# Performance work log

Measured on AMD Instinct MI355X. Metric: run time of the kernel, lower is better.

## Reference

```python
import jax, jax.numpy as jnp
import numpy as np

B, T, C = 4, 2048, 1024
H, HD = 16, 64          # n_heads, head_dim (C = H*HD)
R = 8                   # LoRA rank
SCALING = 16.0 / R      # alpha / r = 2.0


def setup_inputs() -> dict:
    key = jax.random.key(0)
    ks = jax.random.split(key, 16)
    std_a = 1.0 / np.sqrt(R)  # LoRA A init std (B init is zeros in torch; use randn here for a non-trivial baseline)
    inp = {
        "x":  jax.random.normal(ks[0], (B, T, C), dtype=jnp.float32),
        # per-head stacked projection weights [H, C, HD] (bias=False heads)
        "Wq": jax.random.normal(ks[1], (H, C, HD), dtype=jnp.float32) * 0.02,
        "Wk": jax.random.normal(ks[2], (H, C, HD), dtype=jnp.float32) * 0.02,
        "Wv": jax.random.normal(ks[3], (H, C, HD), dtype=jnp.float32) * 0.02,
        # per-head LoRA factors
        "Aq": jax.random.normal(ks[4], (H, C, R), dtype=jnp.float32) * std_a,
        "Bq": jax.random.normal(ks[5], (H, R, HD), dtype=jnp.float32) * 0.02,
        "Ak": jax.random.normal(ks[6], (H, C, R), dtype=jnp.float32) * std_a,
        "Bk": jax.random.normal(ks[7], (H, R, HD), dtype=jnp.float32) * 0.02,
        "Av": jax.random.normal(ks[8], (H, C, R), dtype=jnp.float32) * std_a,
        "Bv": jax.random.normal(ks[9], (H, R, HD), dtype=jnp.float32) * 0.02,
        # output projection C->C with bias, plus LoRA
        "Wp": jax.random.normal(ks[10], (C, C), dtype=jnp.float32) * 0.02,
        "bp": jnp.zeros((C,), dtype=jnp.float32),
        "Ap": jax.random.normal(ks[11], (C, R), dtype=jnp.float32) * std_a,
        "Bp": jax.random.normal(ks[12], (R, C), dtype=jnp.float32) * 0.02,
    }
    return inp


def _lora_proj(x, W, A, Bm):
    # x: [B,T,C]; W: [H,C,HD]; A: [H,C,R]; Bm: [H,R,HD] -> [B,H,T,HD]
    base = jnp.einsum('btc,hcd->bhtd', x, W)
    lora = jnp.einsum('bhtr,hrd->bhtd', jnp.einsum('btc,hcr->bhtr', x, A), Bm)
    return base + SCALING * lora


def reference(x, Wq, Wk, Wv, Aq, Bq, Ak, Bk, Av, Bv, Wp, bp, Ap, Bp):
    Bsz, Tlen, Cdim = x.shape
    q = _lora_proj(x, Wq, Aq, Bq)  # [B,H,T,HD]
    k = _lora_proj(x, Wk, Ak, Bk)
    v = _lora_proj(x, Wv, Av, Bv)

    scores = jnp.einsum('bhtd,bhsd->bhts', q, k) * (HD ** -0.5)  # [B,H,T,T]
    causal = jnp.tril(jnp.ones((Tlen, Tlen), dtype=bool))
    scores = jnp.where(causal, scores, -jnp.inf)
    weights = jax.nn.softmax(scores, axis=-1)  # dropout p=0 (eval) -> no-op

    out = jnp.einsum('bhts,bhsd->bhtd', weights, v)            # [B,H,T,HD]
    out = out.transpose(0, 2, 1, 3).reshape(Bsz, Tlen, Cdim)   # concat heads

    proj = out @ Wp + bp + SCALING * ((out @ Ap) @ Bp)
    return proj
```

## Files before the change

kernel.cpp:

```cpp
#include <hip/hip_runtime.h>
#include <hip/hip_bf16.h>
#include <stdint.h>

typedef __attribute__((ext_vector_type(4))) float f32x4;
typedef __attribute__((ext_vector_type(8))) short bf16x8;

#define LOG2E 1.44269504088896340736f

__device__ __forceinline__ unsigned short f2bf(float f) {
  union { float f; unsigned u; } c; c.f = f;
  unsigned u = c.u + 0x7FFFu + ((c.u >> 16) & 1u);
  return (unsigned short)(u >> 16);
}

__device__ __forceinline__ void gload_lds16(const void* g, void* l) {
  __builtin_amdgcn_global_load_lds((const __attribute__((address_space(1))) void*)g,
                                   (__attribute__((address_space(3))) void*)l, 16, 0, 0);
}

__global__ __launch_bounds__(256) void cast_x_kernel(const float* __restrict__ x,
                                                     unsigned short* __restrict__ o) {
  int i = blockIdx.x * 256 + threadIdx.x;
  const float4* xv = (const float4*)x;
  float4 a = xv[2 * i], b = xv[2 * i + 1];
  union { uint4 v; unsigned short s[8]; } u;
  u.s[0] = f2bf(a.x); u.s[1] = f2bf(a.y); u.s[2] = f2bf(a.z); u.s[3] = f2bf(a.w);
  u.s[4] = f2bf(b.x); u.s[5] = f2bf(b.y); u.s[6] = f2bf(b.z); u.s[7] = f2bf(b.w);
  ((uint4*)o)[i] = u.v;
}

__global__ __launch_bounds__(256) void fold_head_kernel(const float* __restrict__ W,
                                                        const float* __restrict__ A,
                                                        const float* __restrict__ Bm,
                                                        unsigned short* __restrict__ outT,
                                                        float scale) {
  int h = blockIdx.x, cb = blockIdx.y;
  __shared__ float Bs[8][64];
  __shared__ unsigned short tile[64][65];
  int t = threadIdx.x;
  if (t < 128) ((float4*)&Bs[0][0])[t] = ((const float4*)(Bm + (size_t)h * 512))[t];
  __syncthreads();
  int cl = t >> 2;
  int c = cb * 64 + cl;
  int dbase = (t & 3) * 16;
  float4 a0 = *(const float4*)(A + (size_t)h * 8192 + c * 8);
  float4 a1 = *(const float4*)(A + (size_t)h * 8192 + c * 8 + 4);
  const float* Wc = W + (size_t)h * 65536 + (size_t)c * 64;
#pragma unroll
  for (int j = 0; j < 16; ++j) {
    int d = dbase + j;
    float acc = a0.x * Bs[0][d] + a0.y * Bs[1][d] + a0.z * Bs[2][d] + a0.w * Bs[3][d] +
                a1.x * Bs[4][d] + a1.y * Bs[5][d] + a1.z * Bs[6][d] + a1.w * Bs[7][d];
    tile[cl][d] = f2bf(scale * (Wc[d] + 2.0f * acc));
  }
  __syncthreads();
#pragma unroll
  for (int i = 0; i < 16; ++i) {
    int idx = i * 256 + t;
    int d = idx >> 6, c2 = idx & 63;
    outT[(size_t)(h * 64 + d) * 1024 + cb * 64 + c2] = tile[c2][d];
  }
}

__global__ __launch_bounds__(256) void fold_proj_kernel(const float* __restrict__ W,
                                                        const float* __restrict__ A,
                                                        const float* __restrict__ Bm,
                                                        unsigned short* __restrict__ outT) {
  int nb = blockIdx.x, cb = blockIdx.y;
  __shared__ float Bs[8][64];
  __shared__ unsigned short tile[64][65];
  int t = threadIdx.x;
  if (t < 128) {
    int r = t >> 4, dc = t & 15;
    *(float4*)&Bs[r][dc * 4] = *(const float4*)(Bm + (size_t)r * 1024 + nb * 64 + dc * 4);
  }
  __syncthreads();
  int cl = t >> 2;
  int c = cb * 64 + cl;
  int dbase = (t & 3) * 16;
  float4 a0 = *(const float4*)(A + (size_t)c * 8);
  float4 a1 = *(const float4*)(A + (size_t)c * 8 + 4);
  const float* Wc = W + (size_t)c * 1024 + nb * 64;
#pragma unroll
  for (int j = 0; j < 16; ++j) {
    int d = dbase + j;
    float acc = a0.x * Bs[0][d] + a0.y * Bs[1][d] + a0.z * Bs[2][d] + a0.w * Bs[3][d] +
                a1.x * Bs[4][d] + a1.y * Bs[5][d] + a1.z * Bs[6][d] + a1.w * Bs[7][d];
    tile[cl][d] = f2bf(Wc[d] + 2.0f * acc);
  }
  __syncthreads();
#pragma unroll
  for (int i = 0; i < 16; ++i) {
    int idx = i * 256 + t;
    int d = idx >> 6, c2 = idx & 63;
    outT[(size_t)(nb * 64 + d) * 1024 + cb * 64 + c2] = tile[c2][d];
  }
}

template <int MODE>
__global__ __launch_bounds__(512) void gemm256_kernel(const unsigned short* __restrict__ A,
                                                      const unsigned short* __restrict__ B,
                                                      void* __restrict__ Cout,
                                                      const float* __restrict__ bias,
                                                      int M, int N, int K) {
  __shared__ __align__(16) unsigned short lds[2][32768];
  const int t = threadIdx.x;
  const int lane = t & 63;
  const int wid = t >> 6;
  const int wm = wid >> 2, wn = wid & 3;
  const int lr = lane & 15, lg = lane >> 4;
  const int m0 = blockIdx.y * 256, n0 = blockIdx.x * 256;

  f32x4 acc[8][4];
#pragma unroll
  for (int i = 0; i < 8; ++i)
#pragma unroll
    for (int j = 0; j < 4; ++j) acc[i][j] = (f32x4){0.f, 0.f, 0.f, 0.f};

  const int srow = t >> 3;
  const int schk = t & 7;

  auto stage_all = [&](int buf, int kt) {
    const int k0 = kt * 64;
#pragma unroll
    for (int hh = 0; hh < 4; ++hh) {
      const unsigned short* src = (hh < 2) ? A : B;
      const int r0 = ((hh < 2) ? m0 : n0) + (hh & 1) * 128;
      char* dst = (char*)lds[buf] + (hh >= 2 ? 32768 : 0) + (hh & 1) * 16384;
#pragma unroll
      for (int i = 0; i < 2; ++i) {
        int row = i * 64 + srow;
        int gc = schk ^ (row & 7);
        gload_lds16(src + (size_t)(r0 + row) * K + k0 + gc * 8, dst + i * 8192 + t * 16);
      }
    }
  };

  stage_all(0, 0);
  __syncthreads();

  const int NT = K >> 6;
#pragma unroll 1
  for (int kt = 0; kt < NT; ++kt) {
    const int cur = kt & 1;
    const char* Ab = (const char*)lds[cur];
    const char* Bb = (const char*)lds[cur] + 32768;
#pragma unroll
    for (int p = 0; p < 4; ++p) {
      if (p == 0 && kt + 1 < NT) stage_all(cur ^ 1, kt + 1);
      const int mh = p >> 1, nh = p & 1;
#pragma unroll
      for (int kk = 0; kk < 2; ++kk) {
        bf16x8 af[4], bfr[2];
#pragma unroll
        for (int fm = 0; fm < 4; ++fm) {
          int row = wm * 128 + mh * 64 + fm * 16 + lr;
          af[fm] = *(const bf16x8*)(Ab + row * 128 + (((kk * 4 + lg) ^ (row & 7)) * 16));
        }
#pragma unroll
        for (int fn = 0; fn < 2; ++fn) {
          int row = wn * 64 + nh * 32 + fn * 16 + lr;
          bfr[fn] = *(const bf16x8*)(Bb + row * 128 + (((kk * 4 + lg) ^ (row & 7)) * 16));
        }
        __builtin_amdgcn_s_setprio(1);
#pragma unroll
        for (int fm = 0; fm < 4; ++fm)
#pragma unroll
          for (int fn = 0; fn < 2; ++fn)
            acc[mh * 4 + fm][nh * 2 + fn] =
                __builtin_amdgcn_mfma_f32_16x16x32_bf16(af[fm], bfr[fn], acc[mh * 4 + fm][nh * 2 + fn], 0, 0, 0);
        __builtin_amdgcn_s_setprio(0);
      }
    }
    __syncthreads();
  }

#pragma unroll
  for (int fm = 0; fm < 8; ++fm) {
#pragma unroll
    for (int r = 0; r < 4; ++r) {
      int row = m0 + wm * 128 + fm * 16 + lg * 4 + r;
#pragma unroll
      for (int fn = 0; fn < 4; ++fn) {
        int col = n0 + wn * 64 + fn * 16 + lr;
        float v = acc[fm][fn][r];
        if (MODE == 0)
          ((unsigned short*)Cout)[(size_t)row * N + col] = f2bf(v);
        else
          ((float*)Cout)[(size_t)row * N + col] = v + bias[col];
      }
    }
  }
}

__global__ __launch_bounds__(256) void attn_kernel(const unsigned short* __restrict__ qkv,
                                                   const unsigned short* __restrict__ vtb,
                                                   unsigned short* __restrict__ out) {
  __shared__ __align__(16) char kl[2][8192];
  __shared__ __align__(16) char vt[2][8192];
  __shared__ __align__(16) char pl[8192];
  const int t = threadIdx.x;
  const int wid = t >> 6, lane = t & 63;
  const int lr = lane & 15, lg = lane >> 4;
  const int i = blockIdx.x;
  const int xcd = i & 7, s = i >> 3;
  const int bh = xcd + 8 * (s >> 5);
  const int qtile = 31 - (s & 31);
  const int b = bh >> 4, h = bh & 15;
  const size_t baseRow = (size_t)b * 2048;
  const int nkt = qtile + 1;
  const int q0w = qtile * 64 + wid * 16;
  char* pb = pl + wid * 2048;
  const int swP = ((lr & 1) << 4) | ((lr & 12) << 3);
  const int srow = lane >> 3;
  const int sc = lane & 7;

  const unsigned short* qp = qkv + (baseRow + q0w + lr) * 2048 + h * 64 + lg * 8;
  bf16x8 qf0 = *(const bf16x8*)qp;
  bf16x8 qf1 = *(const bf16x8*)(qp + 32);

  f32x4 acc_o[4];
#pragma unroll
  for (int d = 0; d < 4; ++d) acc_o[d] = (f32x4){0.f, 0.f, 0.f, 0.f};
  float l_acc = 0.f;

  const unsigned short* vrow = vtb + (size_t)(h * 64) * 8192 + baseRow;

  auto stage = [&](int kt, int buf) {
#pragma unroll
    for (int ch = 0; ch < 2; ++ch) {
      int kr = ch * 32 + wid * 8 + srow;
      int gc = sc ^ (kr & 7);
      gload_lds16(qkv + (baseRow + kt * 64 + kr) * 2048 + 1024 + h * 64 + gc * 8,
                  &kl[buf][(ch * 256 + t) * 16]);
    }
#pragma unroll
    for (int ch = 0; ch < 2; ++ch) {
      int d = ch * 32 + wid * 8 + srow;
      int gc = sc ^ (((d & 7) ^ (d >> 3)) & 7);
      gload_lds16(vrow + (size_t)d * 8192 + kt * 64 + gc * 8,
                  &vt[buf][(ch * 256 + t) * 16]);
    }
  };

  stage(0, 0);
  __syncthreads();

#pragma unroll 1
  for (int kt = 0; kt < nkt; ++kt) {
    const int cur = kt & 1;
    if (kt + 1 < nkt) stage(kt + 1, cur ^ 1);

    const char* klc = kl[cur];
    f32x4 z[4];
#pragma unroll
    for (int nt = 0; nt < 4; ++nt) {
      int key = nt * 16 + lr;
      const char* kb = klc + key * 128;
      int sw = (key & 7) << 4;
      bf16x8 kf0 = *(const bf16x8*)(kb + ((lg * 16) ^ sw));
      bf16x8 kf1 = *(const bf16x8*)(kb + ((64 + lg * 16) ^ sw));
      f32x4 zz = (f32x4){0.f, 0.f, 0.f, 0.f};
      zz = __builtin_amdgcn_mfma_f32_16x16x32_bf16(kf0, qf0, zz, 0, 0, 0);
      zz = __builtin_amdgcn_mfma_f32_16x16x32_bf16(kf1, qf1, zz, 0, 0, 0);
      z[nt] = zz;
    }
    const bool diag = (kt == qtile);
    const int qg = q0w + lr;
#pragma unroll
    for (int nt = 0; nt < 4; ++nt) {
      union { uint2 v; unsigned short us[4]; } pk;
#pragma unroll
      for (int r = 0; r < 4; ++r) {
        float pv = exp2f(z[nt][r]);
        if (diag) {
          int keyg = kt * 64 + nt * 16 + lg * 4 + r;
          pv = (keyg > qg) ? 0.f : pv;
        }
        l_acc += pv;
        pk.us[r] = f2bf(pv);
      }
      *(uint2*)(pb + lr * 128 + (((nt * 16 + lg * 4) * 2) ^ swP)) = pk.v;
    }
#pragma unroll
    for (int kk = 0; kk < 2; ++kk) {
      bf16x8 pfr = *(const bf16x8*)(pb + lr * 128 + ((kk * 64 + lg * 16) ^ swP));
#pragma unroll
      for (int dt = 0; dt < 4; ++dt) {
        int d = dt * 16 + lr;
        int swv = (((d & 7) ^ ((d >> 3) & 7)) << 4);
        bf16x8 vf = *(const bf16x8*)(vt[cur] + d * 128 + ((kk * 64 + lg * 16) ^ swv));
        acc_o[dt] = __builtin_amdgcn_mfma_f32_16x16x32_bf16(pfr, vf, acc_o[dt], 0, 0, 0);
      }
    }
    __syncthreads();
  }

  float lsum = l_acc;
  lsum += __shfl_xor(lsum, 16);
  lsum += __shfl_xor(lsum, 32);
#pragma unroll
  for (int r = 0; r < 4; ++r) {
    float inv = 1.0f / __shfl(lsum, lg * 4 + r);
    unsigned short* op = out + (baseRow + q0w + lg * 4 + r) * 1024 + h * 64;
#pragma unroll
    for (int dt = 0; dt < 4; ++dt) op[dt * 16 + lr] = f2bf(acc_o[dt][r] * inv);
  }
}

extern "C" void kernel_launch(void* const* d_in, const int* in_sizes, int n_in,
                              void* d_out, int out_size, void* d_ws, size_t ws_size,
                              hipStream_t stream) {
  const float* x = (const float*)d_in[0];
  const float* Wq = (const float*)d_in[1];
  const float* Wk = (const float*)d_in[2];
  const float* Wv = (const float*)d_in[3];
  const float* Aq = (const float*)d_in[4];
  const float* Bq = (const float*)d_in[5];
  const float* Ak = (const float*)d_in[6];
  const float* Bk = (const float*)d_in[7];
  const float* Av = (const float*)d_in[8];
  const float* Bv = (const float*)d_in[9];
  const float* Wp = (const float*)d_in[10];
  const float* bp = (const float*)d_in[11];
  const float* Ap = (const float*)d_in[12];
  const float* Bp = (const float*)d_in[13];

  unsigned short* xb = (unsigned short*)d_ws;
  unsigned short* weff = xb + 8388608;
  unsigned short* weffV = weff + 2097152;
  unsigned short* wpeff = weffV + 1048576;
  unsigned short* qkb = wpeff + 1048576;
  unsigned short* vtb = qkb + 16777216;
  unsigned short* attb = xb;

  cast_x_kernel<<<4096, 256, 0, stream>>>(x, xb);
  dim3 fg(16, 16);
  fold_head_kernel<<<fg, 256, 0, stream>>>(Wq, Aq, Bq, weff, 0.125f * LOG2E);
  fold_head_kernel<<<fg, 256, 0, stream>>>(Wk, Ak, Bk, weff + 1048576, 1.0f);
  fold_head_kernel<<<fg, 256, 0, stream>>>(Wv, Av, Bv, weffV, 1.0f);
  fold_proj_kernel<<<fg, 256, 0, stream>>>(Wp, Ap, Bp, wpeff);

  gemm256_kernel<0><<<dim3(8, 32), 512, 0, stream>>>(xb, weff, (void*)qkb, nullptr, 8192, 2048, 1024);
  gemm256_kernel<0><<<dim3(32, 4), 512, 0, stream>>>(weffV, xb, (void*)vtb, nullptr, 1024, 8192, 1024);
  attn_kernel<<<2048, 256, 0, stream>>>(qkb, vtb, attb);
  gemm256_kernel<1><<<dim3(4, 32), 512, 0, stream>>>(attb, wpeff, d_out, bp, 8192, 1024, 1024);
}
```

Baseline: 329.4 us.

## Template GEMM N-tile width, use MFMA for softmax row sums, packed bf16 convert

The GEMM kernel gains a BN template parameter, so the V-projection and output-projection GEMMs run with 256x128 tiles. This doubles their grid from 128 to 256 blocks and fills more CUs. In attention, the per-lane row-sum accumulation and end-of-kernel shuffles are replaced by an extra MFMA against a ones vector, and the f32 to bf16 packing uses the hardware v_cvt_pk_bf16_f32 instruction. s_setprio hints are also placed around the attention MFMAs. The row sum is now taken from bf16-rounded probabilities, which changes numerics slightly, and the smaller tiles reduce per-block reuse.

```diff
diff --git a/kernel.cpp b/kernel.cpp
--- a/kernel.cpp
+++ b/kernel.cpp
@@ -97,25 +97,28 @@
   }
 }
 
-template <int MODE>
+template <int BN, int MODE>
 __global__ __launch_bounds__(512) void gemm256_kernel(const unsigned short* __restrict__ A,
                                                       const unsigned short* __restrict__ B,
                                                       void* __restrict__ Cout,
                                                       const float* __restrict__ bias,
                                                       int M, int N, int K) {
-  __shared__ __align__(16) unsigned short lds[2][32768];
+  constexpr int WN = BN / 4;
+  constexpr int HN = BN / 8;
+  constexpr int FN = BN / 128;
+  __shared__ __align__(16) char lds[2][(256 + BN) * 128];
   const int t = threadIdx.x;
   const int lane = t & 63;
   const int wid = t >> 6;
   const int wm = wid >> 2, wn = wid & 3;
   const int lr = lane & 15, lg = lane >> 4;
-  const int m0 = blockIdx.y * 256, n0 = blockIdx.x * 256;
-
-  f32x4 acc[8][4];
+  const int m0 = blockIdx.y * 256, n0 = blockIdx.x * BN;
+
+  f32x4 acc[8][2 * FN];
 #pragma unroll
   for (int i = 0; i < 8; ++i)
 #pragma unroll
-    for (int j = 0; j < 4; ++j) acc[i][j] = (f32x4){0.f, 0.f, 0.f, 0.f};
+    for (int j = 0; j < 2 * FN; ++j) acc[i][j] = (f32x4){0.f, 0.f, 0.f, 0.f};
 
   const int srow = t >> 3;
   const int schk = t & 7;
@@ -123,17 +126,23 @@
   auto stage_all = [&](int buf, int kt) {
     const int k0 = kt * 64;
 #pragma unroll
-    for (int hh = 0; hh < 4; ++hh) {
-      const unsigned short* src = (hh < 2) ? A : B;
-      const int r0 = ((hh < 2) ? m0 : n0) + (hh & 1) * 128;
-      char* dst = (char*)lds[buf] + (hh >= 2 ? 32768 : 0) + (hh & 1) * 16384;
-#pragma unroll
-      for (int i = 0; i < 2; ++i) {
-        int row = i * 64 + srow;
+    for (int g = 0; g < 2; ++g)
+#pragma unroll
+      for (int i2 = 0; i2 < 2; ++i2) {
+        int row = i2 * 64 + srow;
         int gc = schk ^ (row & 7);
-        gload_lds16(src + (size_t)(r0 + row) * K + k0 + gc * 8, dst + i * 8192 + t * 16);
-      }
-    }
+        gload_lds16(A + (size_t)(m0 + g * 128 + row) * K + k0 + gc * 8,
+                    lds[buf] + g * 16384 + i2 * 8192 + t * 16);
+      }
+#pragma unroll
+    for (int g = 0; g < BN / 128; ++g)
+#pragma unroll
+      for (int i2 = 0; i2 < 2; ++i2) {
+        int row = i2 * 64 + srow;
+        int gc = schk ^ (row & 7);
+        gload_lds16(B + (size_t)(n0 + g * 128 + row) * K + k0 + gc * 8,
+                    lds[buf] + 32768 + g * 16384 + i2 * 8192 + t * 16);
+      }
   };
 
   stage_all(0, 0);
@@ -151,24 +160,24 @@
       const int mh = p >> 1, nh = p & 1;
 #pragma unroll
       for (int kk = 0; kk < 2; ++kk) {
-        bf16x8 af[4], bfr[2];
+        bf16x8 af[4], bfr[FN];
 #pragma unroll
         for (int fm = 0; fm < 4; ++fm) {
           int row = wm * 128 + mh * 64 + fm * 16 + lr;
           af[fm] = *(const bf16x8*)(Ab + row * 128 + (((kk * 4 + lg) ^ (row & 7)) * 16));
         }
 #pragma unroll
-        for (int fn = 0; fn < 2; ++fn) {
-          int row = wn * 64 + nh * 32 + fn * 16 + lr;
+        for (int fn = 0; fn < FN; ++fn) {
+          int row = wn * WN + nh * HN + fn * 16 + lr;
           bfr[fn] = *(const bf16x8*)(Bb + row * 128 + (((kk * 4 + lg) ^ (row & 7)) * 16));
         }
         __builtin_amdgcn_s_setprio(1);
 #pragma unroll
         for (int fm = 0; fm < 4; ++fm)
 #pragma unroll
-          for (int fn = 0; fn < 2; ++fn)
-            acc[mh * 4 + fm][nh * 2 + fn] =
-                __builtin_amdgcn_mfma_f32_16x16x32_bf16(af[fm], bfr[fn], acc[mh * 4 + fm][nh * 2 + fn], 0, 0, 0);
+          for (int fn = 0; fn < FN; ++fn)
+            acc[mh * 4 + fm][nh * FN + fn] =
+                __builtin_amdgcn_mfma_f32_16x16x32_bf16(af[fm], bfr[fn], acc[mh * 4 + fm][nh * FN + fn], 0, 0, 0);
         __builtin_amdgcn_s_setprio(0);
       }
     }
@@ -181,8 +190,8 @@
     for (int r = 0; r < 4; ++r) {
       int row = m0 + wm * 128 + fm * 16 + lg * 4 + r;
 #pragma unroll
-      for (int fn = 0; fn < 4; ++fn) {
-        int col = n0 + wn * 64 + fn * 16 + lr;
+      for (int fn = 0; fn < 2 * FN; ++fn) {
+        int col = n0 + wn * WN + fn * 16 + lr;
         float v = acc[fm][fn][r];
         if (MODE == 0)
           ((unsigned short*)Cout)[(size_t)row * N + col] = f2bf(v);
@@ -219,10 +228,13 @@
   bf16x8 qf0 = *(const bf16x8*)qp;
   bf16x8 qf1 = *(const bf16x8*)(qp + 32);
 
+  const bf16x8 onesf = {(short)0x3F80, (short)0x3F80, (short)0x3F80, (short)0x3F80,
+                        (short)0x3F80, (short)0x3F80, (short)0x3F80, (short)0x3F80};
+
   f32x4 acc_o[4];
 #pragma unroll
   for (int d = 0; d < 4; ++d) acc_o[d] = (f32x4){0.f, 0.f, 0.f, 0.f};
-  float l_acc = 0.f;
+  f32x4 acc_l = (f32x4){0.f, 0.f, 0.f, 0.f};
 
   const unsigned short* vrow = vtb + (size_t)(h * 64) * 8192 + baseRow;
 
@@ -261,30 +273,38 @@
       bf16x8 kf0 = *(const bf16x8*)(kb + ((lg * 16) ^ sw));
       bf16x8 kf1 = *(const bf16x8*)(kb + ((64 + lg * 16) ^ sw));
       f32x4 zz = (f32x4){0.f, 0.f, 0.f, 0.f};
+      __builtin_amdgcn_s_setprio(1);
       zz = __builtin_amdgcn_mfma_f32_16x16x32_bf16(kf0, qf0, zz, 0, 0, 0);
       zz = __builtin_amdgcn_mfma_f32_16x16x32_bf16(kf1, qf1, zz, 0, 0, 0);
+      __builtin_amdgcn_s_setprio(0);
       z[nt] = zz;
     }
     const bool diag = (kt == qtile);
     const int qg = q0w + lr;
 #pragma unroll
     for (int nt = 0; nt < 4; ++nt) {
-      union { uint2 v; unsigned short us[4]; } pk;
+      float pv[4];
 #pragma unroll
       for (int r = 0; r < 4; ++r) {
-        float pv = exp2f(z[nt][r]);
+        float e = exp2f(z[nt][r]);
         if (diag) {
           int keyg = kt * 64 + nt * 16 + lg * 4 + r;
-          pv = (keyg > qg) ? 0.f : pv;
+          e = (keyg > qg) ? 0.f : e;
         }
-        l_acc += pv;
-        pk.us[r] = f2bf(pv);
-      }
-      *(uint2*)(pb + lr * 128 + (((nt * 16 + lg * 4) * 2) ^ swP)) = pk.v;
+        pv[r] = e;
+      }
+      unsigned w0, w1;
+      asm("v_cvt_pk_bf16_f32 %0, %1, %2" : "=v"(w0) : "v"(pv[0]), "v"(pv[1]));
+      asm("v_cvt_pk_bf16_f32 %0, %1, %2" : "=v"(w1) : "v"(pv[2]), "v"(pv[3]));
+      uint2 pk2;
+      pk2.x = w0;
+      pk2.y = w1;
+      *(uint2*)(pb + lr * 128 + (((nt * 16 + lg * 4) * 2) ^ swP)) = pk2;
     }
 #pragma unroll
     for (int kk = 0; kk < 2; ++kk) {
       bf16x8 pfr = *(const bf16x8*)(pb + lr * 128 + ((kk * 64 + lg * 16) ^ swP));
+      __builtin_amdgcn_s_setprio(1);
 #pragma unroll
       for (int dt = 0; dt < 4; ++dt) {
         int d = dt * 16 + lr;
@@ -292,16 +312,15 @@
         bf16x8 vf = *(const bf16x8*)(vt[cur] + d * 128 + ((kk * 64 + lg * 16) ^ swv));
         acc_o[dt] = __builtin_amdgcn_mfma_f32_16x16x32_bf16(pfr, vf, acc_o[dt], 0, 0, 0);
       }
+      acc_l = __builtin_amdgcn_mfma_f32_16x16x32_bf16(pfr, onesf, acc_l, 0, 0, 0);
+      __builtin_amdgcn_s_setprio(0);
     }
     __syncthreads();
   }
 
-  float lsum = l_acc;
-  lsum += __shfl_xor(lsum, 16);
-  lsum += __shfl_xor(lsum, 32);
 #pragma unroll
   for (int r = 0; r < 4; ++r) {
-    float inv = 1.0f / __shfl(lsum, lg * 4 + r);
+    float inv = 1.0f / acc_l[r];
     unsigned short* op = out + (baseRow + q0w + lg * 4 + r) * 1024 + h * 64;
 #pragma unroll
     for (int dt = 0; dt < 4; ++dt) op[dt * 16 + lr] = f2bf(acc_o[dt][r] * inv);
@@ -341,8 +360,8 @@
   fold_head_kernel<<<fg, 256, 0, stream>>>(Wv, Av, Bv, weffV, 1.0f);
   fold_proj_kernel<<<fg, 256, 0, stream>>>(Wp, Ap, Bp, wpeff);
 
-  gemm256_kernel<0><<<dim3(8, 32), 512, 0, stream>>>(xb, weff, (void*)qkb, nullptr, 8192, 2048, 1024);
-  gemm256_kernel<0><<<dim3(32, 4), 512, 0, stream>>>(weffV, xb, (void*)vtb, nullptr, 1024, 8192, 1024);
+  gemm256_kernel<256, 0><<<dim3(8, 32), 512, 0, stream>>>(xb, weff, (void*)qkb, nullptr, 8192, 2048, 1024);
+  gemm256_kernel<128, 0><<<dim3(64, 4), 512, 0, stream>>>(weffV, xb, (void*)vtb, nullptr, 1024, 8192, 1024);
   attn_kernel<<<2048, 256, 0, stream>>>(qkb, vtb, attb);
-  gemm256_kernel<1><<<dim3(4, 32), 512, 0, stream>>>(attb, wpeff, d_out, bp, 8192, 1024, 1024);
-}
+  gemm256_kernel<128, 1><<<dim3(8, 32), 512, 0, stream>>>(attb, wpeff, d_out, bp, 8192, 1024, 1024);
+}
```

Measured after the change: 304.1 us. 1.08x faster.
